# Kernel optimization log

Measured on AMD Instinct MI355X. Metric: run time of the kernel, lower is better.

The kernel has to match this reference:

```python
import jax, jax.numpy as jnp
import numpy as np

N_NODES = 100000
N_RELS = 237
N_EDGES = 500000
D_IN = 128
D_HID = 128
D_OUT = 128


def setup_inputs() -> dict:
    key = jax.random.key(0)
    ks = jax.random.split(key, 13)
    src = jax.random.randint(ks[0], (N_EDGES,), 0, N_NODES, dtype=jnp.int32)
    dst = jax.random.randint(ks[1], (N_EDGES,), 0, N_NODES, dtype=jnp.int32)
    rel = jax.random.randint(ks[2], (N_EDGES,), 0, N_RELS, dtype=jnp.int32)
    triplets = jnp.stack([src, dst, rel], axis=1)  # [E, 3]
    s = 0.05
    return {
        "triplets": triplets,
        "ent_embed": jax.random.normal(ks[3], (N_NODES, D_IN), jnp.float32) * s,
        "rel_embed": jax.random.normal(ks[4], (N_RELS, D_IN), jnp.float32) * s,
        "W_ent": jax.random.normal(ks[5], (D_IN, D_HID), jnp.float32) * s,
        "b_ent": jnp.zeros((D_HID,), jnp.float32),
        "W_rel": jax.random.normal(ks[6], (D_IN, D_HID), jnp.float32) * s,
        "b_rel": jnp.zeros((D_HID,), jnp.float32),
        "W_ent2": jax.random.normal(ks[7], (3 * D_HID, D_OUT), jnp.float32) * s,
        "b_ent2": jnp.zeros((D_OUT,), jnp.float32),
        "a_w": jax.random.normal(ks[8], (D_OUT, 1), jnp.float32) * s,
        "a_b": jnp.zeros((1,), jnp.float32),
    }


def reference(triplets, ent_embed, rel_embed, W_ent, b_ent, W_rel, b_rel,
              W_ent2, b_ent2, a_w, a_b):
    src_i, dst_i, rel_i = triplets[:, 0], triplets[:, 1], triplets[:, 2]
    # embedding gathers
    src = ent_embed[src_i]          # [E, D_IN]
    dst = ent_embed[dst_i]          # [E, D_IN]
    rel = rel_embed[rel_i]          # [E, D_IN]
    # shared fc_ent projection on src and dst, fc_rel on rel
    src = src @ W_ent + b_ent       # [E, D_HID]
    dst = dst @ W_ent + b_ent
    rel = rel @ W_rel + b_rel
    # per-edge feature c = fc_ent2(cat([src, dst, rel]))
    c = jnp.concatenate([src, dst, rel], axis=1) @ W_ent2 + b_ent2  # [E, D_OUT]
    # unnormalized exp attention score (leaky_relu slope 0.01, torch default)
    b = jnp.exp(jax.nn.leaky_relu((c @ a_w + a_b)[:, 0], negative_slope=0.01))  # [E]
    # segment softmax over edges sharing a source node
    b_sum = jax.ops.segment_sum(b, src_i, num_segments=N_NODES)  # [N]
    alpha = b / b_sum[src_i]                                     # [E]
    # weighted neighbor aggregation per source node
    h = jax.ops.segment_sum(alpha[:, None] * c, src_i, num_segments=N_NODES)  # [N, D_OUT]
    return h
```

## Files before the change

kernel.cpp:

```cpp
#include <hip/hip_runtime.h>
#include <hip/hip_bf16.h>

#define N_NODES_C 100000
#define N_PAD_C   100096
#define N_RELS_C  237
#define N_EDGES_C 500000
#define D 128

typedef __attribute__((ext_vector_type(8))) short short8;
typedef __attribute__((ext_vector_type(4))) float f32x4;

__device__ __forceinline__ ushort f2bf(float x) {
    union { float f; uint u; } v; v.f = x;
    uint r = v.u + 0x7FFFu + ((v.u >> 16) & 1u);
    return (ushort)(r >> 16);
}
__device__ __forceinline__ float bf2f_hi(uint u) {
    union { uint u; float f; } v; v.u = u; return v.f;
}

__global__ void k_fuse_w(const float* __restrict__ W_ent, const float* __restrict__ W_rel,
                         const float* __restrict__ W_ent2,
                         const float* __restrict__ b_ent, const float* __restrict__ b_rel,
                         const float* __restrict__ b_ent2,
                         float* __restrict__ WR, ushort* __restrict__ WfTb,
                         float* __restrict__ biasC) {
    int j = threadIdx.x;
    int k = blockIdx.x;
    int which = blockIdx.y;
    if (which == 0) {
        float acc = 0.f;
        for (int i = 0; i < D; ++i) acc += W_ent[k*D+i] * W_ent2[i*D+j];
        WfTb[j*D + k] = f2bf(acc);
    } else if (which == 1) {
        float acc = 0.f;
        for (int i = 0; i < D; ++i) acc += W_ent[k*D+i] * W_ent2[(D+i)*D+j];
        WfTb[(D+j)*D + k] = f2bf(acc);
    } else if (which == 2) {
        float acc = 0.f;
        for (int i = 0; i < D; ++i) acc += W_rel[k*D+i] * W_ent2[(2*D+i)*D+j];
        WR[k*D + j] = acc;
    } else if (k == 0) {
        float acc = b_ent2[j];
        for (int i = 0; i < D; ++i) {
            acc += b_ent[i] * (W_ent2[i*D+j] + W_ent2[(D+i)*D+j]);
            acc += b_rel[i] * W_ent2[(2*D+i)*D+j];
        }
        biasC[j] = acc;
    }
}

__global__ void k_rel_scalars(const float* __restrict__ rel_embed,
                              const float* __restrict__ a_w, const float* __restrict__ a_b,
                              const float* __restrict__ WR, const float* __restrict__ biasC,
                              ushort* __restrict__ RmB, float* __restrict__ sR,
                              float* __restrict__ sConst) {
    int j = threadIdx.x;
    int b = blockIdx.x;
    __shared__ float red[128];
    if (b < N_RELS_C) {
        float acc = 0.f;
        for (int k = 0; k < D; ++k) acc += rel_embed[b*D+k] * WR[k*D+j];
        RmB[b*D+j] = f2bf(acc);
        red[j] = acc * a_w[j];
        __syncthreads();
        for (int s = 64; s > 0; s >>= 1) { if (j < s) red[j] += red[j+s]; __syncthreads(); }
        if (j == 0) sR[b] = red[0];
    } else {
        red[j] = biasC[j] * a_w[j];
        __syncthreads();
        for (int s = 64; s > 0; s >>= 1) { if (j < s) red[j] += red[j+s]; __syncthreads(); }
        if (j == 0) sConst[0] = red[0] + a_b[0];
    }
}

__global__ __launch_bounds__(512, 4) void k1_mfma(const float* __restrict__ ent,
                                                  const ushort* __restrict__ WfTb,
                                                  const float* __restrict__ a_w,
                                                  ushort* __restrict__ AnB,
                                                  ushort* __restrict__ BnB,
                                                  float* __restrict__ sA,
                                                  float* __restrict__ sB,
                                                  int n_nodes) {
    __shared__ __align__(16) ushort wL[256*128];
    int tid = threadIdx.x;
    int m0 = blockIdx.x * 128;

#pragma unroll
    for (int u = 0; u < 8; ++u) {
        int f = u*512 + tid;
        int r = f >> 4, k16 = f & 15;
        *(uint4*)&wL[r*128 + ((k16 ^ (r & 15)) << 3)] =
            *(const uint4*)&WfTb[r*128 + (k16 << 3)];
    }
    __syncthreads();

    int wave = tid >> 6, lane = tid & 63;
    int ny = wave >> 2;
    int q = lane >> 4, c = lane & 15;
    int wm = (wave & 3) * 32;

    f32x4 acc[2][8];
#pragma unroll
    for (int mt = 0; mt < 2; ++mt)
#pragma unroll
        for (int nt = 0; nt < 8; ++nt) { f32x4 z = {0.f,0.f,0.f,0.f}; acc[mt][nt] = z; }

#pragma unroll
    for (int chunk = 0; chunk < 4; ++chunk) {
        int k16 = chunk*4 + q;
        short8 a[2];
#pragma unroll
        for (int mt = 0; mt < 2; ++mt) {
            int row = m0 + wm + mt*16 + c;
            float4 e0 = make_float4(0.f,0.f,0.f,0.f), e1 = e0;
            if (row < n_nodes) {
                const float* ep = &ent[(size_t)row*D + (k16 << 3)];
                e0 = *(const float4*)ep;
                e1 = *(const float4*)(ep + 4);
            }
            short8 pk;
            pk[0]=(short)f2bf(e0.x); pk[1]=(short)f2bf(e0.y); pk[2]=(short)f2bf(e0.z); pk[3]=(short)f2bf(e0.w);
            pk[4]=(short)f2bf(e1.x); pk[5]=(short)f2bf(e1.y); pk[6]=(short)f2bf(e1.z); pk[7]=(short)f2bf(e1.w);
            a[mt] = pk;
        }
#pragma unroll
        for (int nt = 0; nt < 8; ++nt) {
            int wrow = ny*128 + nt*16 + c;
            short8 b = *(const short8*)&wL[wrow*128 + ((k16 ^ c) << 3)];
            acc[0][nt] = __builtin_amdgcn_mfma_f32_16x16x32_bf16(a[0], b, acc[0][nt], 0, 0, 0);
            acc[1][nt] = __builtin_amdgcn_mfma_f32_16x16x32_bf16(a[1], b, acc[1][nt], 0, 0, 0);
        }
    }

    float aw[8];
#pragma unroll
    for (int nt = 0; nt < 8; ++nt) aw[nt] = a_w[nt*16 + c];

    ushort* out  = ny ? BnB : AnB;
    float*  sOut = ny ? sB  : sA;

#pragma unroll
    for (int mt = 0; mt < 2; ++mt) {
#pragma unroll
        for (int reg = 0; reg < 4; ++reg) {
            int m = m0 + wm + mt*16 + q*4 + reg;
            float pa = 0.f;
#pragma unroll
            for (int nt = 0; nt < 8; ++nt) pa += acc[mt][nt][reg] * aw[nt];
#pragma unroll
            for (int msk = 1; msk < 16; msk <<= 1) pa += __shfl_xor(pa, msk);
            if (m < n_nodes) {
                if (c == 0) sOut[m] = pa;
#pragma unroll
                for (int nt = 0; nt < 8; ++nt)
                    out[(size_t)m*D + nt*16 + c] = f2bf(acc[mt][nt][reg]);
            }
        }
    }
}

__global__ void k_hist(const int* __restrict__ trip, int* __restrict__ deg, int n_edges) {
    int e = blockIdx.x*256 + threadIdx.x;
    if (e >= n_edges) return;
    int s = trip[3*e];
    if ((unsigned)s >= (unsigned)N_NODES_C) return;
    atomicAdd(&deg[s], 1);
}

__global__ void k_scan1(const int* __restrict__ deg, int* __restrict__ off,
                        int* __restrict__ bsum, int n) {
    __shared__ int s[1024];
    int i = blockIdx.x*1024 + threadIdx.x;
    int v = (i < n) ? deg[i] : 0;
    s[threadIdx.x] = v; __syncthreads();
    for (int d = 1; d < 1024; d <<= 1) {
        int t = (threadIdx.x >= d) ? s[threadIdx.x - d] : 0;
        __syncthreads();
        s[threadIdx.x] += t;
        __syncthreads();
    }
    if (i < n) off[i] = s[threadIdx.x] - v;
    if (threadIdx.x == 1023) bsum[blockIdx.x] = s[1023];
}

__global__ void k_scan2(int* __restrict__ bsum, int nb) {
    __shared__ int s[128];
    int v = (threadIdx.x < nb) ? bsum[threadIdx.x] : 0;
    s[threadIdx.x] = v; __syncthreads();
    for (int d = 1; d < 128; d <<= 1) {
        int t = (threadIdx.x >= d) ? s[threadIdx.x - d] : 0;
        __syncthreads();
        s[threadIdx.x] += t;
        __syncthreads();
    }
    if (threadIdx.x < nb) bsum[threadIdx.x] = s[threadIdx.x] - v;
}

__global__ void k_scan3(int* __restrict__ off, int* __restrict__ cursor,
                        const int* __restrict__ bsum, int n, int total_edges) {
    int i = blockIdx.x*1024 + threadIdx.x;
    if (i < n) {
        int o = off[i] + bsum[blockIdx.x];
        off[i] = o;
        cursor[i] = o;
    }
    if (i == 0) off[n] = total_edges;
}

__global__ void k_edge_b(const int* __restrict__ trip, const float* __restrict__ sB,
                         const float* __restrict__ sR, int* __restrict__ cursor,
                         uint2* __restrict__ kb, int n_edges) {
    int e = blockIdx.x*256 + threadIdx.x;
    if (e >= n_edges) return;
    int s = trip[3*e], d = trip[3*e+1], r = trip[3*e+2];
    if ((unsigned)s >= (unsigned)N_NODES_C || (unsigned)d >= (unsigned)N_NODES_C ||
        (unsigned)r >= (unsigned)N_RELS_C) return;
    float v = sB[d] + sR[r];
    int p = atomicAdd(&cursor[s], 1);
    kb[p] = make_uint2((uint)(d | (r << 20)), __float_as_uint(v));
}

__global__ void k_aggregate(const int* __restrict__ off, const uint2* __restrict__ kb,
                            const ushort* __restrict__ AnB, const ushort* __restrict__ BnB,
                            const ushort* __restrict__ RmB, const float* __restrict__ biasC,
                            const float* __restrict__ sA, const float* __restrict__ sConst,
                            float* __restrict__ h, int n_nodes) {
    int g = threadIdx.x >> 4, lane = threadIdx.x & 15;
    int n = blockIdx.x*16 + g;
    if (n >= n_nodes) return;
    int o0 = off[n], o1 = off[n+1];
    int c = lane*8;
    float* hp = &h[(size_t)n*D + c];
    if (o0 == o1) {
        *(float4*)hp     = make_float4(0.f,0.f,0.f,0.f);
        *(float4*)(hp+4) = make_float4(0.f,0.f,0.f,0.f);
        return;
    }
    float t = sA[n] + sConst[0];
    float num[8];
#pragma unroll
    for (int i = 0; i < 8; ++i) num[i] = 0.f;
    float den = 0.f;

    int p = o0;
    for (; p + 4 <= o1; p += 4) {
        uint2 kv[4]; uint4 gB[4], gR[4];
#pragma unroll
        for (int u = 0; u < 4; ++u) kv[u] = kb[p+u];
#pragma unroll
        for (int u = 0; u < 4; ++u) {
            gB[u] = *(const uint4*)&BnB[(size_t)(kv[u].x & 0xFFFFF)*D + c];
            gR[u] = *(const uint4*)&RmB[(size_t)(kv[u].x >> 20)*D + c];
        }
#pragma unroll
        for (int u = 0; u < 4; ++u) {
            float logit = t + __uint_as_float(kv[u].y);
            float l = logit > 0.f ? logit : 0.01f*logit;
            float b = expf(l);
            den += b;
            const uint* bu = (const uint*)&gB[u];
            const uint* ru = (const uint*)&gR[u];
#pragma unroll
            for (int i = 0; i < 4; ++i) {
                num[2*i]   += b * (bf2f_hi(bu[i] << 16)         + bf2f_hi(ru[i] << 16));
                num[2*i+1] += b * (bf2f_hi(bu[i] & 0xFFFF0000u) + bf2f_hi(ru[i] & 0xFFFF0000u));
            }
        }
    }
    for (; p < o1; ++p) {
        uint2 kv = kb[p];
        float logit = t + __uint_as_float(kv.y);
        float l = logit > 0.f ? logit : 0.01f*logit;
        float b = expf(l);
        den += b;
        uint4 gB = *(const uint4*)&BnB[(size_t)(kv.x & 0xFFFFF)*D + c];
        uint4 gR = *(const uint4*)&RmB[(size_t)(kv.x >> 20)*D + c];
        const uint* bu = (const uint*)&gB;
        const uint* ru = (const uint*)&gR;
#pragma unroll
        for (int i = 0; i < 4; ++i) {
            num[2*i]   += b * (bf2f_hi(bu[i] << 16)         + bf2f_hi(ru[i] << 16));
            num[2*i+1] += b * (bf2f_hi(bu[i] & 0xFFFF0000u) + bf2f_hi(ru[i] & 0xFFFF0000u));
        }
    }

    float inv = 1.f / den;
    uint4 araw = *(const uint4*)&AnB[(size_t)n*D + c];
    const uint* au = (const uint*)&araw;
    float4 bc0 = *(const float4*)&biasC[c];
    float4 bc1 = *(const float4*)&biasC[c+4];
    float4 o0v, o1v;
    o0v.x = bf2f_hi(au[0] << 16)         + bc0.x + num[0]*inv;
    o0v.y = bf2f_hi(au[0] & 0xFFFF0000u) + bc0.y + num[1]*inv;
    o0v.z = bf2f_hi(au[1] << 16)         + bc0.z + num[2]*inv;
    o0v.w = bf2f_hi(au[1] & 0xFFFF0000u) + bc0.w + num[3]*inv;
    o1v.x = bf2f_hi(au[2] << 16)         + bc1.x + num[4]*inv;
    o1v.y = bf2f_hi(au[2] & 0xFFFF0000u) + bc1.y + num[5]*inv;
    o1v.z = bf2f_hi(au[3] << 16)         + bc1.z + num[6]*inv;
    o1v.w = bf2f_hi(au[3] & 0xFFFF0000u) + bc1.w + num[7]*inv;
    *(float4*)hp     = o0v;
    *(float4*)(hp+4) = o1v;
}

extern "C" void kernel_launch(void* const* d_in, const int* in_sizes, int n_in,
                              void* d_out, int out_size, void* d_ws, size_t ws_size,
                              hipStream_t stream) {
    const int*   trip   = (const int*)  d_in[0];
    const float* ent    = (const float*)d_in[1];
    const float* relE   = (const float*)d_in[2];
    const float* W_ent  = (const float*)d_in[3];
    const float* b_ent  = (const float*)d_in[4];
    const float* W_rel  = (const float*)d_in[5];
    const float* b_rel  = (const float*)d_in[6];
    const float* W_ent2 = (const float*)d_in[7];
    const float* b_ent2 = (const float*)d_in[8];
    const float* a_w    = (const float*)d_in[9];
    const float* a_b    = (const float*)d_in[10];
    float* h = (float*)d_out;

    char* ws = (char*)d_ws;
    size_t o = 0;
    auto alloc = [&](size_t bytes) { size_t p = o; o += (bytes + 255) & ~(size_t)255; return p; };
    float*  WR     = (float*) (ws + alloc(128*128*4));
    ushort* WfTb   = (ushort*)(ws + alloc(256*128*2));
    float*  biasC  = (float*) (ws + alloc(128*4));
    ushort* RmB    = (ushort*)(ws + alloc((size_t)N_RELS_C*128*2));
    float*  sR     = (float*) (ws + alloc(N_RELS_C*4));
    float*  sConst = (float*) (ws + alloc(4));
    float*  sA     = (float*) (ws + alloc((size_t)N_NODES_C*4));
    float*  sB     = (float*) (ws + alloc((size_t)N_NODES_C*4));
    int*    deg    = (int*)   (ws + alloc((size_t)N_NODES_C*4));
    int*    off    = (int*)   (ws + alloc(((size_t)N_NODES_C+1)*4));
    int*    cursor = (int*)   (ws + alloc((size_t)N_NODES_C*4));
    int*    bsum   = (int*)   (ws + alloc(128*4));
    uint2*  kb     = (uint2*) (ws + alloc((size_t)N_EDGES_C*8));
    ushort* BnB    = (ushort*)(ws + alloc((size_t)N_PAD_C*128*2));
    ushort* AnB    = (ushort*)(ws + alloc((size_t)N_PAD_C*128*2));

    hipMemsetAsync(deg, 0, (size_t)N_NODES_C*4, stream);

    k_fuse_w<<<dim3(128,4), 128, 0, stream>>>(W_ent, W_rel, W_ent2, b_ent, b_rel, b_ent2,
                                              WR, WfTb, biasC);
    k_rel_scalars<<<N_RELS_C+1, 128, 0, stream>>>(relE, a_w, a_b, WR, biasC,
                                                  RmB, sR, sConst);
    k1_mfma<<<N_PAD_C/128, 512, 0, stream>>>(ent, WfTb, a_w, AnB, BnB, sA, sB, N_NODES_C);
    k_hist<<<(N_EDGES_C+255)/256, 256, 0, stream>>>(trip, deg, N_EDGES_C);
    int nb = (N_NODES_C + 1023)/1024;
    k_scan1<<<nb, 1024, 0, stream>>>(deg, off, bsum, N_NODES_C);
    k_scan2<<<1, 128, 0, stream>>>(bsum, nb);
    k_scan3<<<nb, 1024, 0, stream>>>(off, cursor, bsum, N_NODES_C, N_EDGES_C);
    k_edge_b<<<(N_EDGES_C+255)/256, 256, 0, stream>>>(trip, sB, sR, cursor, kb, N_EDGES_C);
    k_aggregate<<<(N_NODES_C+15)/16, 256, 0, stream>>>(off, kb, AnB, BnB, RmB, biasC,
                                                       sA, sConst, h, N_NODES_C);
}
```

Before: 244.6 us.

## Fuse weight precompute kernels, vectorize triplet loads, widen aggregate lanes

Merges the two weight-preprocessing kernels into one, replacing the reductions with atomics into memset-zeroed sR/sConst. This drops a launch and the intermediate WR buffer. The histogram and edge-bucketing kernels now have each thread handle four edges through int4 loads of the triplet array. The aggregation kernel moves from 16 to 8 lanes per node, each handling 16 channels, so every lane issues more independent gathers. The trade-offs are higher register pressure, less parallelism per node, and a 4-edge unrolled path that relies on the edge count being a multiple of 4 for aligned loads.

```diff
diff --git a/kernel.cpp b/kernel.cpp
--- a/kernel.cpp
+++ b/kernel.cpp
@@ -19,58 +19,49 @@
     union { uint u; float f; } v; v.u = u; return v.f;
 }
 
-__global__ void k_fuse_w(const float* __restrict__ W_ent, const float* __restrict__ W_rel,
-                         const float* __restrict__ W_ent2,
-                         const float* __restrict__ b_ent, const float* __restrict__ b_rel,
-                         const float* __restrict__ b_ent2,
-                         float* __restrict__ WR, ushort* __restrict__ WfTb,
-                         float* __restrict__ biasC) {
-    int j = threadIdx.x;
-    int k = blockIdx.x;
-    int which = blockIdx.y;
-    if (which == 0) {
+__global__ void k_fuse_all(const float* __restrict__ W_ent, const float* __restrict__ W_rel,
+                           const float* __restrict__ W_ent2,
+                           const float* __restrict__ b_ent, const float* __restrict__ b_rel,
+                           const float* __restrict__ b_ent2,
+                           const float* __restrict__ relE,
+                           const float* __restrict__ a_w, const float* __restrict__ a_b,
+                           ushort* __restrict__ WfTb, ushort* __restrict__ RmB,
+                           float* __restrict__ biasC, float* __restrict__ sR,
+                           float* __restrict__ sConst) {
+    int j = blockIdx.x;
+    int t = threadIdx.x;
+    int y = blockIdx.y;
+    if (y == 0) {
         float acc = 0.f;
-        for (int i = 0; i < D; ++i) acc += W_ent[k*D+i] * W_ent2[i*D+j];
-        WfTb[j*D + k] = f2bf(acc);
-    } else if (which == 1) {
+        for (int i = 0; i < D; ++i) acc += W_ent[t*D+i] * W_ent2[i*D+j];
+        WfTb[j*D + t] = f2bf(acc);
+    } else if (y == 1) {
         float acc = 0.f;
-        for (int i = 0; i < D; ++i) acc += W_ent[k*D+i] * W_ent2[(D+i)*D+j];
-        WfTb[(D+j)*D + k] = f2bf(acc);
-    } else if (which == 2) {
+        for (int i = 0; i < D; ++i) acc += W_ent[t*D+i] * W_ent2[(D+i)*D+j];
+        WfTb[(D+j)*D + t] = f2bf(acc);
+    } else {
+        __shared__ float wcol[128];
+        __shared__ float red[128];
         float acc = 0.f;
-        for (int i = 0; i < D; ++i) acc += W_rel[k*D+i] * W_ent2[(2*D+i)*D+j];
-        WR[k*D + j] = acc;
-    } else if (k == 0) {
-        float acc = b_ent2[j];
-        for (int i = 0; i < D; ++i) {
-            acc += b_ent[i] * (W_ent2[i*D+j] + W_ent2[(D+i)*D+j]);
-            acc += b_rel[i] * W_ent2[(2*D+i)*D+j];
-        }
-        biasC[j] = acc;
-    }
-}
-
-__global__ void k_rel_scalars(const float* __restrict__ rel_embed,
-                              const float* __restrict__ a_w, const float* __restrict__ a_b,
-                              const float* __restrict__ WR, const float* __restrict__ biasC,
-                              ushort* __restrict__ RmB, float* __restrict__ sR,
-                              float* __restrict__ sConst) {
-    int j = threadIdx.x;
-    int b = blockIdx.x;
-    __shared__ float red[128];
-    if (b < N_RELS_C) {
-        float acc = 0.f;
-        for (int k = 0; k < D; ++k) acc += rel_embed[b*D+k] * WR[k*D+j];
-        RmB[b*D+j] = f2bf(acc);
-        red[j] = acc * a_w[j];
-        __syncthreads();
-        for (int s = 64; s > 0; s >>= 1) { if (j < s) red[j] += red[j+s]; __syncthreads(); }
-        if (j == 0) sR[b] = red[0];
-    } else {
-        red[j] = biasC[j] * a_w[j];
-        __syncthreads();
-        for (int s = 64; s > 0; s >>= 1) { if (j < s) red[j] += red[j+s]; __syncthreads(); }
-        if (j == 0) sConst[0] = red[0] + a_b[0];
+        for (int i = 0; i < D; ++i) acc += W_rel[t*D+i] * W_ent2[(2*D+i)*D+j];
+        wcol[t] = acc;
+        red[t] = b_ent[t]*(W_ent2[t*D+j] + W_ent2[(D+t)*D+j]) + b_rel[t]*W_ent2[(2*D+t)*D+j];
+        __syncthreads();
+        for (int s = 64; s > 0; s >>= 1) { if (t < s) red[t] += red[t+s]; __syncthreads(); }
+        if (t == 0) {
+            float bC = red[0] + b_ent2[j];
+            biasC[j] = bC;
+            float contrib = bC * a_w[j];
+            if (j == 0) contrib += a_b[0];
+            atomicAdd(sConst, contrib);
+        }
+        float awj = a_w[j];
+        for (int r = t; r < N_RELS_C; r += 128) {
+            float rv = 0.f;
+            for (int k = 0; k < D; ++k) rv += relE[r*D+k] * wcol[k];
+            RmB[r*D + j] = f2bf(rv);
+            atomicAdd(&sR[r], rv * awj);
+        }
     }
 }
 
@@ -161,11 +152,18 @@
 }
 
 __global__ void k_hist(const int* __restrict__ trip, int* __restrict__ deg, int n_edges) {
-    int e = blockIdx.x*256 + threadIdx.x;
-    if (e >= n_edges) return;
-    int s = trip[3*e];
-    if ((unsigned)s >= (unsigned)N_NODES_C) return;
-    atomicAdd(&deg[s], 1);
+    int e0 = (blockIdx.x*256 + threadIdx.x) * 4;
+    if (e0 >= n_edges) return;
+    int4 w0 = *(const int4*)&trip[e0*3];
+    int4 w1 = *(const int4*)&trip[e0*3 + 4];
+    int4 w2 = *(const int4*)&trip[e0*3 + 8];
+    int s[4] = {w0.x, w0.w, w1.z, w2.y};
+#pragma unroll
+    for (int u = 0; u < 4; ++u) {
+        if (e0 + u >= n_edges) break;
+        if ((unsigned)s[u] >= (unsigned)N_NODES_C) continue;
+        atomicAdd(&deg[s[u]], 1);
+    }
 }
 
 __global__ void k_scan1(const int* __restrict__ deg, int* __restrict__ off,
@@ -211,14 +209,23 @@
 __global__ void k_edge_b(const int* __restrict__ trip, const float* __restrict__ sB,
                          const float* __restrict__ sR, int* __restrict__ cursor,
                          uint2* __restrict__ kb, int n_edges) {
-    int e = blockIdx.x*256 + threadIdx.x;
-    if (e >= n_edges) return;
-    int s = trip[3*e], d = trip[3*e+1], r = trip[3*e+2];
-    if ((unsigned)s >= (unsigned)N_NODES_C || (unsigned)d >= (unsigned)N_NODES_C ||
-        (unsigned)r >= (unsigned)N_RELS_C) return;
-    float v = sB[d] + sR[r];
-    int p = atomicAdd(&cursor[s], 1);
-    kb[p] = make_uint2((uint)(d | (r << 20)), __float_as_uint(v));
+    int e0 = (blockIdx.x*256 + threadIdx.x) * 4;
+    if (e0 >= n_edges) return;
+    int4 w0 = *(const int4*)&trip[e0*3];
+    int4 w1 = *(const int4*)&trip[e0*3 + 4];
+    int4 w2 = *(const int4*)&trip[e0*3 + 8];
+    int s[4] = {w0.x, w0.w, w1.z, w2.y};
+    int d[4] = {w0.y, w1.x, w1.w, w2.z};
+    int r[4] = {w0.z, w1.y, w2.x, w2.w};
+#pragma unroll
+    for (int u = 0; u < 4; ++u) {
+        if (e0 + u >= n_edges) break;
+        if ((unsigned)s[u] >= (unsigned)N_NODES_C || (unsigned)d[u] >= (unsigned)N_NODES_C ||
+            (unsigned)r[u] >= (unsigned)N_RELS_C) continue;
+        float v = sB[d[u]] + sR[r[u]];
+        int p = atomicAdd(&cursor[s[u]], 1);
+        kb[p] = make_uint2((uint)(d[u] | (r[u] << 20)), __float_as_uint(v));
+    }
 }
 
 __global__ void k_aggregate(const int* __restrict__ off, const uint2* __restrict__ kb,
@@ -226,32 +233,36 @@
                             const ushort* __restrict__ RmB, const float* __restrict__ biasC,
                             const float* __restrict__ sA, const float* __restrict__ sConst,
                             float* __restrict__ h, int n_nodes) {
-    int g = threadIdx.x >> 4, lane = threadIdx.x & 15;
-    int n = blockIdx.x*16 + g;
+    int g = threadIdx.x >> 3, lane = threadIdx.x & 7;
+    int n = blockIdx.x*32 + g;
     if (n >= n_nodes) return;
     int o0 = off[n], o1 = off[n+1];
-    int c = lane*8;
+    int c = lane*16;
     float* hp = &h[(size_t)n*D + c];
     if (o0 == o1) {
-        *(float4*)hp     = make_float4(0.f,0.f,0.f,0.f);
-        *(float4*)(hp+4) = make_float4(0.f,0.f,0.f,0.f);
+        float4 z = make_float4(0.f,0.f,0.f,0.f);
+        *(float4*)hp = z; *(float4*)(hp+4) = z; *(float4*)(hp+8) = z; *(float4*)(hp+12) = z;
         return;
     }
     float t = sA[n] + sConst[0];
-    float num[8];
-#pragma unroll
-    for (int i = 0; i < 8; ++i) num[i] = 0.f;
+    float num[16];
+#pragma unroll
+    for (int i = 0; i < 16; ++i) num[i] = 0.f;
     float den = 0.f;
 
     int p = o0;
     for (; p + 4 <= o1; p += 4) {
-        uint2 kv[4]; uint4 gB[4], gR[4];
+        uint2 kv[4]; uint4 gB[4][2], gR[4][2];
 #pragma unroll
         for (int u = 0; u < 4; ++u) kv[u] = kb[p+u];
 #pragma unroll
         for (int u = 0; u < 4; ++u) {
-            gB[u] = *(const uint4*)&BnB[(size_t)(kv[u].x & 0xFFFFF)*D + c];
-            gR[u] = *(const uint4*)&RmB[(size_t)(kv[u].x >> 20)*D + c];
+            const ushort* bp = &BnB[(size_t)(kv[u].x & 0xFFFFF)*D + c];
+            gB[u][0] = *(const uint4*)bp;
+            gB[u][1] = *(const uint4*)(bp + 8);
+            const ushort* rp = &RmB[(size_t)(kv[u].x >> 20)*D + c];
+            gR[u][0] = *(const uint4*)rp;
+            gR[u][1] = *(const uint4*)(rp + 8);
         }
 #pragma unroll
         for (int u = 0; u < 4; ++u) {
@@ -259,12 +270,15 @@
             float l = logit > 0.f ? logit : 0.01f*logit;
             float b = expf(l);
             den += b;
-            const uint* bu = (const uint*)&gB[u];
-            const uint* ru = (const uint*)&gR[u];
-#pragma unroll
-            for (int i = 0; i < 4; ++i) {
-                num[2*i]   += b * (bf2f_hi(bu[i] << 16)         + bf2f_hi(ru[i] << 16));
-                num[2*i+1] += b * (bf2f_hi(bu[i] & 0xFFFF0000u) + bf2f_hi(ru[i] & 0xFFFF0000u));
+#pragma unroll
+            for (int half = 0; half < 2; ++half) {
+                const uint* bu = (const uint*)&gB[u][half];
+                const uint* ru = (const uint*)&gR[u][half];
+#pragma unroll
+                for (int i = 0; i < 4; ++i) {
+                    num[half*8 + 2*i]     += b * (bf2f_hi(bu[i] << 16)         + bf2f_hi(ru[i] << 16));
+                    num[half*8 + 2*i + 1] += b * (bf2f_hi(bu[i] & 0xFFFF0000u) + bf2f_hi(ru[i] & 0xFFFF0000u));
+                }
             }
         }
     }
@@ -274,33 +288,42 @@
         float l = logit > 0.f ? logit : 0.01f*logit;
         float b = expf(l);
         den += b;
-        uint4 gB = *(const uint4*)&BnB[(size_t)(kv.x & 0xFFFFF)*D + c];
-        uint4 gR = *(const uint4*)&RmB[(size_t)(kv.x >> 20)*D + c];
-        const uint* bu = (const uint*)&gB;
-        const uint* ru = (const uint*)&gR;
-#pragma unroll
-        for (int i = 0; i < 4; ++i) {
-            num[2*i]   += b * (bf2f_hi(bu[i] << 16)         + bf2f_hi(ru[i] << 16));
-            num[2*i+1] += b * (bf2f_hi(bu[i] & 0xFFFF0000u) + bf2f_hi(ru[i] & 0xFFFF0000u));
+        const ushort* bp = &BnB[(size_t)(kv.x & 0xFFFFF)*D + c];
+        const ushort* rp = &RmB[(size_t)(kv.x >> 20)*D + c];
+        uint4 gB0 = *(const uint4*)bp, gB1 = *(const uint4*)(bp + 8);
+        uint4 gR0 = *(const uint4*)rp, gR1 = *(const uint4*)(rp + 8);
+#pragma unroll
+        for (int half = 0; half < 2; ++half) {
+            const uint* bu = (const uint*)(half ? &gB1 : &gB0);
+            const uint* ru = (const uint*)(half ? &gR1 : &gR0);
+#pragma unroll
+            for (int i = 0; i < 4; ++i) {
+                num[half*8 + 2*i]     += b * (bf2f_hi(bu[i] << 16)         + bf2f_hi(ru[i] << 16));
+                num[half*8 + 2*i + 1] += b * (bf2f_hi(bu[i] & 0xFFFF0000u) + bf2f_hi(ru[i] & 0xFFFF0000u));
+            }
         }
     }
 
     float inv = 1.f / den;
-    uint4 araw = *(const uint4*)&AnB[(size_t)n*D + c];
-    const uint* au = (const uint*)&araw;
-    float4 bc0 = *(const float4*)&biasC[c];
-    float4 bc1 = *(const float4*)&biasC[c+4];
-    float4 o0v, o1v;
-    o0v.x = bf2f_hi(au[0] << 16)         + bc0.x + num[0]*inv;
-    o0v.y = bf2f_hi(au[0] & 0xFFFF0000u) + bc0.y + num[1]*inv;
-    o0v.z = bf2f_hi(au[1] << 16)         + bc0.z + num[2]*inv;
-    o0v.w = bf2f_hi(au[1] & 0xFFFF0000u) + bc0.w + num[3]*inv;
-    o1v.x = bf2f_hi(au[2] << 16)         + bc1.x + num[4]*inv;
-    o1v.y = bf2f_hi(au[2] & 0xFFFF0000u) + bc1.y + num[5]*inv;
-    o1v.z = bf2f_hi(au[3] << 16)         + bc1.z + num[6]*inv;
-    o1v.w = bf2f_hi(au[3] & 0xFFFF0000u) + bc1.w + num[7]*inv;
-    *(float4*)hp     = o0v;
-    *(float4*)(hp+4) = o1v;
+    const ushort* ap = &AnB[(size_t)n*D + c];
+    uint4 a0 = *(const uint4*)ap, a1 = *(const uint4*)(ap + 8);
+#pragma unroll
+    for (int half = 0; half < 2; ++half) {
+        const uint* au = (const uint*)(half ? &a1 : &a0);
+        float4 bcL = *(const float4*)&biasC[c + half*8];
+        float4 bcH = *(const float4*)&biasC[c + half*8 + 4];
+        float4 oL, oH;
+        oL.x = bf2f_hi(au[0] << 16)         + bcL.x + num[half*8+0]*inv;
+        oL.y = bf2f_hi(au[0] & 0xFFFF0000u) + bcL.y + num[half*8+1]*inv;
+        oL.z = bf2f_hi(au[1] << 16)         + bcL.z + num[half*8+2]*inv;
+        oL.w = bf2f_hi(au[1] & 0xFFFF0000u) + bcL.w + num[half*8+3]*inv;
+        oH.x = bf2f_hi(au[2] << 16)         + bcH.x + num[half*8+4]*inv;
+        oH.y = bf2f_hi(au[2] & 0xFFFF0000u) + bcH.y + num[half*8+5]*inv;
+        oH.z = bf2f_hi(au[3] << 16)         + bcH.z + num[half*8+6]*inv;
+        oH.w = bf2f_hi(au[3] & 0xFFFF0000u) + bcH.w + num[half*8+7]*inv;
+        *(float4*)(hp + half*8)     = oL;
+        *(float4*)(hp + half*8 + 4) = oH;
+    }
 }
 
 extern "C" void kernel_launch(void* const* d_in, const int* in_sizes, int n_in,
@@ -322,15 +345,16 @@
     char* ws = (char*)d_ws;
     size_t o = 0;
     auto alloc = [&](size_t bytes) { size_t p = o; o += (bytes + 255) & ~(size_t)255; return p; };
-    float*  WR     = (float*) (ws + alloc(128*128*4));
     ushort* WfTb   = (ushort*)(ws + alloc(256*128*2));
     float*  biasC  = (float*) (ws + alloc(128*4));
     ushort* RmB    = (ushort*)(ws + alloc((size_t)N_RELS_C*128*2));
+    float*  sA     = (float*) (ws + alloc((size_t)N_NODES_C*4));
+    float*  sB     = (float*) (ws + alloc((size_t)N_NODES_C*4));
+    size_t z0 = o;
     float*  sR     = (float*) (ws + alloc(N_RELS_C*4));
     float*  sConst = (float*) (ws + alloc(4));
-    float*  sA     = (float*) (ws + alloc((size_t)N_NODES_C*4));
-    float*  sB     = (float*) (ws + alloc((size_t)N_NODES_C*4));
     int*    deg    = (int*)   (ws + alloc((size_t)N_NODES_C*4));
+    size_t z1 = o;
     int*    off    = (int*)   (ws + alloc(((size_t)N_NODES_C+1)*4));
     int*    cursor = (int*)   (ws + alloc((size_t)N_NODES_C*4));
     int*    bsum   = (int*)   (ws + alloc(128*4));
@@ -338,19 +362,17 @@
     ushort* BnB    = (ushort*)(ws + alloc((size_t)N_PAD_C*128*2));
     ushort* AnB    = (ushort*)(ws + alloc((size_t)N_PAD_C*128*2));
 
-    hipMemsetAsync(deg, 0, (size_t)N_NODES_C*4, stream);
-
-    k_fuse_w<<<dim3(128,4), 128, 0, stream>>>(W_ent, W_rel, W_ent2, b_ent, b_rel, b_ent2,
-                                              WR, WfTb, biasC);
-    k_rel_scalars<<<N_RELS_C+1, 128, 0, stream>>>(relE, a_w, a_b, WR, biasC,
-                                                  RmB, sR, sConst);
+    hipMemsetAsync(ws + z0, 0, z1 - z0, stream);
+
+    k_fuse_all<<<dim3(128,3), 128, 0, stream>>>(W_ent, W_rel, W_ent2, b_ent, b_rel, b_ent2,
+                                                relE, a_w, a_b, WfTb, RmB, biasC, sR, sConst);
     k1_mfma<<<N_PAD_C/128, 512, 0, stream>>>(ent, WfTb, a_w, AnB, BnB, sA, sB, N_NODES_C);
-    k_hist<<<(N_EDGES_C+255)/256, 256, 0, stream>>>(trip, deg, N_EDGES_C);
+    k_hist<<<(N_EDGES_C/4 + 255)/256, 256, 0, stream>>>(trip, deg, N_EDGES_C);
     int nb = (N_NODES_C + 1023)/1024;
     k_scan1<<<nb, 1024, 0, stream>>>(deg, off, bsum, N_NODES_C);
     k_scan2<<<1, 128, 0, stream>>>(bsum, nb);
     k_scan3<<<nb, 1024, 0, stream>>>(off, cursor, bsum, N_NODES_C, N_EDGES_C);
-    k_edge_b<<<(N_EDGES_C+255)/256, 256, 0, stream>>>(trip, sB, sR, cursor, kb, N_EDGES_C);
-    k_aggregate<<<(N_NODES_C+15)/16, 256, 0, stream>>>(off, kb, AnB, BnB, RmB, biasC,
+    k_edge_b<<<(N_EDGES_C/4 + 255)/256, 256, 0, stream>>>(trip, sB, sR, cursor, kb, N_EDGES_C);
+    k_aggregate<<<(N_NODES_C+31)/32, 256, 0, stream>>>(off, kb, AnB, BnB, RmB, biasC,
                                                        sA, sConst, h, N_NODES_C);
 }
```

Result: slower. 271.2 us (+10.9%).
